# Optimization experiments

Hardware: AMD Instinct MI355X
Metric: run time of the kernel (lower is better)

## Reference

```python
import jax, jax.numpy as jnp
import numpy as np
from jax import lax

B, L_IN, DEC_LEN = 1024, 2048, 64
H = 128            # hidden_size
CARD, EMB = 200, 16  # categorical feature cardinality / embedding dim
VDIM = 4
IN_SIZE = EMB + 1 + 1  # cat-embed + continuous feat (Linear(1,1)) + target value


def setup_inputs() -> dict:
    key = jax.random.key(0)
    k = jax.random.split(key, 19)
    s = 1.0 / np.sqrt(H)  # torch LSTM/Linear default init scale
    u = lambda kk, shape: jax.random.uniform(kk, shape, minval=-s, maxval=s, dtype=jnp.float32)
    return {
        "cat_in": jax.random.randint(k[0], (B, L_IN), 0, CARD, dtype=jnp.int32),
        "cont_in": jax.random.normal(k[1], (B, L_IN, 1), dtype=jnp.float32),
        "X_in": jax.random.normal(k[2], (B, L_IN, 1), dtype=jnp.float32),
        "cat_out": jax.random.randint(k[3], (B, DEC_LEN), 0, CARD, dtype=jnp.int32),
        "cont_out": jax.random.normal(k[4], (B, DEC_LEN, 1), dtype=jnp.float32),
        # learned params
        "emb_table": jax.random.normal(k[5], (CARD, EMB), dtype=jnp.float32) * 0.02,
        "cont_w": jax.random.normal(k[6], (1, 1), dtype=jnp.float32) * 0.5,  # Linear(1,1,bias=False)
        "Wih_e": u(k[7], (4 * H, IN_SIZE)),
        "Whh_e": u(k[8], (4 * H, H)),
        "b_e": u(k[9], (4 * H,)),   # b_ih + b_hh folded together
        "Wih_d": u(k[10], (4 * H, IN_SIZE)),
        "Whh_d": u(k[11], (4 * H, H)),
        "b_d": u(k[12], (4 * H,)),
        "Wm": u(k[13], (1, H)), "bm": u(k[14], (1,)),
        "Ws": u(k[15], (1, H)), "bs": u(k[16], (1,)),
        "Wv": u(k[17], (VDIM, H)), "bv": u(k[18], (VDIM,)),
    }


def _lstm_cell(x, h, c, Wih, Whh, b):
    # torch gate order: i, f, g, o
    gates = x @ Wih.T + h @ Whh.T + b  # [B, 4H]
    i, f, g, o = jnp.split(gates, 4, axis=-1)
    c_new = jax.nn.sigmoid(f) * c + jax.nn.sigmoid(i) * jnp.tanh(g)
    h_new = jax.nn.sigmoid(o) * jnp.tanh(c_new)
    return h_new, c_new


def reference(cat_in, cont_in, X_in, cat_out, cont_out, emb_table, cont_w,
              Wih_e, Whh_e, b_e, Wih_d, Whh_d, b_d, Wm, bm, Ws, bs, Wv, bv):
    w00 = cont_w[0, 0]
    # feature embedding: Embedding for categorical, Linear(1,1,no bias) for continuous
    feats_in_embed = jnp.concatenate([emb_table[cat_in], cont_in * w00], axis=-1)  # [B,L,EMB+1]
    enc_in = jnp.concatenate([feats_in_embed, X_in], axis=-1)                      # [B,L,IN_SIZE]

    h0 = jnp.zeros((X_in.shape[0], H), dtype=X_in.dtype)

    def enc_step(carry, xt):
        h, c = carry
        return _lstm_cell(xt, h, c, Wih_e, Whh_e, b_e), None

    # encoder outputs are unused downstream; only the final (h, c) state matters
    (h, c), _ = lax.scan(enc_step, (h0, h0), jnp.swapaxes(enc_in, 0, 1))

    feats_out_embed = jnp.concatenate([emb_table[cat_out], cont_out * w00], axis=-1)  # [B,D,EMB+1]

    def dec_step(carry, feats_next):
        h, c, x_prev, f_prev = carry
        xt = jnp.concatenate([f_prev, x_prev], axis=-1)  # [B, IN_SIZE]
        h, c = _lstm_cell(xt, h, c, Wih_d, Whh_d, b_d)
        mu = h @ Wm.T + bm                     # [B,1]
        std = jax.nn.softplus(h @ Ws.T + bs)   # [B,1]
        v = h @ Wv.T + bv                      # [B,VDIM]
        return (h, c, mu, feats_next), (mu, std, v)

    init = (h, c, X_in[:, -1, :], feats_in_embed[:, -1, :])
    _, (means, stds, vs) = lax.scan(dec_step, init, jnp.swapaxes(feats_out_embed, 0, 1))
    # [D,B,*] -> [B,D,*]
    return (jnp.swapaxes(means, 0, 1), jnp.swapaxes(stds, 0, 1), jnp.swapaxes(vs, 0, 1))
```

## Files before the change

### kernel.cpp

```cpp
#include <hip/hip_runtime.h>
#include <math.h>

typedef _Float16 half8 __attribute__((ext_vector_type(8)));
typedef float float4v __attribute__((ext_vector_type(4)));

constexpr int Lc   = 2048;
constexpr int DECc = 64;
constexpr int Hc   = 128;
constexpr int EMBc = 16;
constexpr int INc  = 18;
constexpr int NBc  = 4;
constexpr int NTc  = 512;
constexpr int CARD = 200;
constexpr int ZS   = 160;


__device__ __forceinline__ float rcp_(float x) { return __builtin_amdgcn_rcpf(x); }
__device__ __forceinline__ float sigm(float x) { return rcp_(1.0f + __expf(-x)); }
__device__ __forceinline__ float tanh_(float x) { return 2.0f * rcp_(1.0f + __expf(-2.0f * x)) - 1.0f; }
__device__ __forceinline__ float softplus_(float x) { return __logf(1.0f + __expf(x)); }

__device__ __forceinline__ float sel4(float4v v, int q) {
    const float a = (q & 1) ? v[1] : v[0];
    const float b = (q & 1) ? v[3] : v[2];
    return (q & 2) ? b : a;
}


__global__ __launch_bounds__(NTc, 1) void rnnar_kernel(
    const int*   __restrict__ cat_in,  const float* __restrict__ cont_in,
    const float* __restrict__ X_in,    const int*   __restrict__ cat_out,
    const float* __restrict__ cont_out,const float* __restrict__ emb_table,
    const float* __restrict__ cont_w,
    const float* __restrict__ Wih_e, const float* __restrict__ Whh_e, const float* __restrict__ b_e,
    const float* __restrict__ Wih_d, const float* __restrict__ Whh_d, const float* __restrict__ b_d,
    const float* __restrict__ Wm, const float* __restrict__ bm,
    const float* __restrict__ Ws, const float* __restrict__ bs,
    const float* __restrict__ Wv, const float* __restrict__ bv,
    float* __restrict__ out)
{
    __shared__ _Float16      z_lds[2][NBc * ZS];
    __shared__ _Float16      emb_lds[CARD * EMBc];
    __shared__ _Float16      xs0[NBc * Lc];
    __shared__ _Float16      xs1[NBc * Lc];
    __shared__ _Float16      xo_lds[NBc * DECc];
    __shared__ unsigned char catb[NBc * Lc];
    __shared__ unsigned char catob[NBc * DECc];
    __shared__ float         h32_lds[NBc * 132];
    __shared__ float         wh_lds[6 * Hc];
    __shared__ float         hb_lds[8];
    __shared__ float         mu_lds[4];

    const int tid  = threadIdx.x;
    const int lane = tid & 63;
    const int wv   = tid >> 6;
    const int q    = lane >> 4;
    const int col  = lane & 15;
    const int cell = 16 * wv + col;
    const int bx   = col & 3;
    const int b0   = blockIdx.x * NBc;
    const float w00 = cont_w[0];

    {
        int* z32 = (int*)&z_lds[0][0];
        for (int i = tid; i < NBc * ZS; i += NTc) z32[i] = 0;
    }
    for (int i = tid; i < NBc * Lc; i += NTc) {
        const int b = i >> 11, t = i & (Lc - 1);
        catb[i] = (unsigned char)cat_in[(b0 + b) * Lc + t];
        xs0[i]  = (_Float16)(cont_in[(b0 + b) * Lc + t] * w00);
        xs1[i]  = (_Float16)(X_in[(b0 + b) * Lc + t]);
    }
    if (tid < NBc * DECc) {
        const int b = tid >> 6, t = tid & 63;
        catob[tid]  = (unsigned char)cat_out[(b0 + b) * DECc + t];
        xo_lds[tid] = (_Float16)(cont_out[(b0 + b) * DECc + t] * w00);
    }
    for (int i = tid; i < CARD * EMBc; i += NTc) emb_lds[i] = (_Float16)emb_table[i];
    for (int i = tid; i < 6 * Hc; i += NTc) {
        const int o = i >> 7, k = i & 127;
        wh_lds[i] = (o == 0) ? Wm[k] : (o == 1) ? Ws[k] : Wv[(o - 2) * Hc + k];
    }
    if (tid == 0) { hb_lds[0] = bm[0]; hb_lds[1] = bs[0]; }
    if (tid < 4)  { hb_lds[2 + tid] = bv[tid]; mu_lds[tid] = 0.0f; }

    half8 Bf[4][5];
    float bias_s[4];
    float w17_s[4];
    #define LOAD_T(WIH, WHH, BB)                                               \
    {                                                                          \
        _Pragma("unroll")                                                      \
        for (int gt = 0; gt < 4; ++gt) {                                       \
            const int row = gt * Hc + cell;                                    \
            _Pragma("unroll")                                                  \
            for (int kt = 0; kt < 5; ++kt) {                                   \
                half8 f;                                                       \
                _Pragma("unroll")                                              \
                for (int j = 0; j < 8; ++j) {                                  \
                    const int k = 32 * kt + 8 * q + j;                         \
                    float v = 0.0f;                                            \
                    if (k < Hc)             v = WHH[row * Hc + k];             \
                    else if (k < Hc + INc)  v = WIH[row * INc + (k - Hc)];     \
                    f[j] = (_Float16)v;                                        \
                }                                                              \
                Bf[gt][kt] = f;                                                \
            }                                                                  \
            bias_s[gt] = BB[row];                                              \
            w17_s[gt]  = WIH[row * INc + 17];                                  \
        }                                                                      \
    }

    LOAD_T(Wih_e, Whh_e, b_e);
    __syncthreads();

    float4v acc_pre[4];

    #define PRE_ENC(T1)                                                        \
    {                                                                          \
        const int t1 = (T1);                                                   \
        half8 ax;                                                              \
        _Pragma("unroll") for (int j = 0; j < 8; ++j) ax[j] = (_Float16)0.0f;  \
        if (q < 2)       ax = *(const half8*)&emb_lds[(int)catb[bx * Lc + t1] * EMBc + 8 * q]; \
        else if (q == 2) { ax[0] = xs0[bx * Lc + t1]; ax[1] = xs1[bx * Lc + t1]; } \
        _Pragma("unroll")                                                      \
        for (int gt = 0; gt < 4; ++gt) {                                       \
            float4v a = {bias_s[gt], bias_s[gt], bias_s[gt], bias_s[gt]};      \
            acc_pre[gt] = __builtin_amdgcn_mfma_f32_16x16x32_f16(ax, Bf[gt][4], a, 0, 0, 0); \
        }                                                                      \
    }

    PRE_ENC(0);

    int p = 0;
    float c_reg = 0.f;

    for (int t = 0; t < Lc; ++t) {
        const _Float16* zr = &z_lds[p][0];
        _Float16*       zw = &z_lds[p ^ 1][0];

        const _Float16* ap = zr + bx * ZS + 8 * q;
        half8 Az[4];
        #pragma unroll
        for (int kt = 0; kt < 4; ++kt) Az[kt] = *(const half8*)(ap + 32 * kt);

        float4v acc[4];
        #pragma unroll
        for (int gt = 0; gt < 4; ++gt) {
            float4v a = acc_pre[gt];
            #pragma unroll
            for (int kt = 0; kt < 4; ++kt)
                a = __builtin_amdgcn_mfma_f32_16x16x32_f16(Az[kt], Bf[gt][kt], a, 0, 0, 0);
            acc[gt] = a;
        }

        PRE_ENC((t + 1 < Lc) ? t + 1 : Lc - 1);

        const float gi = sel4(acc[0], q);
        const float gf = sel4(acc[1], q);
        const float gg = sel4(acc[2], q);
        const float go = sel4(acc[3], q);

        const float cn = sigm(gf) * c_reg + sigm(gi) * tanh_(gg);
        c_reg = cn;
        zw[q * ZS + cell] = (_Float16)(sigm(go) * tanh_(cn));

        __syncthreads();
        p ^= 1;
    }

    LOAD_T(Wih_d, Whh_d, b_d);
    const float bm0 = hb_lds[0], bs0 = hb_lds[1];

    {
        const int t1 = Lc - 1;
        half8 ax;
        #pragma unroll
        for (int j = 0; j < 8; ++j) ax[j] = (_Float16)0.0f;
        if (q < 2)       ax = *(const half8*)&emb_lds[(int)catb[bx * Lc + t1] * EMBc + 8 * q];
        else if (q == 2) { ax[0] = xs0[bx * Lc + t1]; ax[1] = xs1[bx * Lc + t1]; }
        #pragma unroll
        for (int gt = 0; gt < 4; ++gt) {
            float4v a = {bias_s[gt], bias_s[gt], bias_s[gt], bias_s[gt]};
            acc_pre[gt] = __builtin_amdgcn_mfma_f32_16x16x32_f16(ax, Bf[gt][4], a, 0, 0, 0);
        }
    }
    __syncthreads();

    for (int t = 0; t < DECc; ++t) {
        const _Float16* zr = &z_lds[p][0];
        _Float16*       zw = &z_lds[p ^ 1][0];

        const float muq = mu_lds[q];

        const _Float16* ap = zr + bx * ZS + 8 * q;
        half8 Az[4];
        #pragma unroll
        for (int kt = 0; kt < 4; ++kt) Az[kt] = *(const half8*)(ap + 32 * kt);

        float4v acc[4];
        #pragma unroll
        for (int gt = 0; gt < 4; ++gt) {
            float4v a = acc_pre[gt];
            #pragma unroll
            for (int kt = 0; kt < 4; ++kt)
                a = __builtin_amdgcn_mfma_f32_16x16x32_f16(Az[kt], Bf[gt][kt], a, 0, 0, 0);
            acc[gt] = a;
        }

        {
            half8 ax;
            #pragma unroll
            for (int j = 0; j < 8; ++j) ax[j] = (_Float16)0.0f;
            if (q < 2)       ax = *(const half8*)&emb_lds[(int)catob[bx * DECc + t] * EMBc + 8 * q];
            else if (q == 2) ax[0] = xo_lds[bx * DECc + t];
            #pragma unroll
            for (int gt = 0; gt < 4; ++gt) {
                float4v a = {bias_s[gt], bias_s[gt], bias_s[gt], bias_s[gt]};
                acc_pre[gt] = __builtin_amdgcn_mfma_f32_16x16x32_f16(ax, Bf[gt][4], a, 0, 0, 0);
            }
        }

        const float gi = sel4(acc[0], q) + muq * w17_s[0];
        const float gf = sel4(acc[1], q) + muq * w17_s[1];
        const float gg = sel4(acc[2], q) + muq * w17_s[2];
        const float go = sel4(acc[3], q) + muq * w17_s[3];

        const float cn = sigm(gf) * c_reg + sigm(gi) * tanh_(gg);
        c_reg = cn;
        const float hv = sigm(go) * tanh_(cn);
        zw[q * ZS + cell] = (_Float16)hv;
        h32_lds[q * 132 + cell] = hv;

        __syncthreads();

        if (tid < 384) {
            const int grp = tid >> 4;
            const int l16 = tid & 15;
            const int b   = grp & 3, o = grp >> 2;
            float s = 0.0f;
            #pragma unroll
            for (int j = 0; j < 8; ++j) {
                const int k = l16 + 16 * j;
                s += wh_lds[o * Hc + k] * h32_lds[b * 132 + k];
            }
            s += __shfl_xor(s, 1);
            s += __shfl_xor(s, 2);
            s += __shfl_xor(s, 4);
            s += __shfl_xor(s, 8);
            if (l16 == 0) {
                const int gb = b0 + b;
                if (o == 0) {
                    const float mu = s + bm0;
                    out[gb * DECc + t] = mu;
                    mu_lds[b] = mu;
                } else if (o == 1) {
                    out[65536 + gb * DECc + t] = softplus_(s + bs0);
                } else {
                    out[131072 + (gb * DECc + t) * 4 + (o - 2)] = s + hb_lds[2 + (o - 2)];
                }
            }
        }
        __syncthreads();
        p ^= 1;
    }
    #undef LOAD_T
    #undef PRE_ENC
}

extern "C" void kernel_launch(void* const* d_in, const int* in_sizes, int n_in,
                              void* d_out, int out_size, void* d_ws, size_t ws_size,
                              hipStream_t stream) {
    rnnar_kernel<<<1024 / NBc, NTc, 0, stream>>>(
        (const int*)d_in[0],   (const float*)d_in[1],  (const float*)d_in[2],
        (const int*)d_in[3],   (const float*)d_in[4],  (const float*)d_in[5],
        (const float*)d_in[6],
        (const float*)d_in[7], (const float*)d_in[8],  (const float*)d_in[9],
        (const float*)d_in[10],(const float*)d_in[11], (const float*)d_in[12],
        (const float*)d_in[13],(const float*)d_in[14],
        (const float*)d_in[15],(const float*)d_in[16],
        (const float*)d_in[17],(const float*)d_in[18],
        (float*)d_out);
}
```

Measured before the change: 1.380 ms.

## Stream encoder inputs from global and batch input projections over four timesteps

Drops the up-front staging of the whole 2048-step input sequence into shared memory. Each wave now loads the inputs for four future timesteps from global memory during the loop. One MFMA per gate computes the input-plus-bias projections for four steps by four batches, which are stashed in a small LDS buffer and read back each step. This is meant to shrink the long prologue, the LDS footprint and the per-step input MFMA work. In exchange, global-load latency now sits inside the serial recurrence with only one step of prefetch distance.

```diff
diff --git a/kernel.cpp b/kernel.cpp
--- a/kernel.cpp
+++ b/kernel.cpp
@@ -25,7 +25,6 @@
     const float b = (q & 1) ? v[3] : v[2];
     return (q & 2) ? b : a;
 }
-
 
 __global__ __launch_bounds__(NTc, 1) void rnnar_kernel(
     const int*   __restrict__ cat_in,  const float* __restrict__ cont_in,
@@ -41,15 +40,13 @@
 {
     __shared__ _Float16      z_lds[2][NBc * ZS];
     __shared__ _Float16      emb_lds[CARD * EMBc];
-    __shared__ _Float16      xs0[NBc * Lc];
-    __shared__ _Float16      xs1[NBc * Lc];
-    __shared__ _Float16      xo_lds[NBc * DECc];
-    __shared__ unsigned char catb[NBc * Lc];
-    __shared__ unsigned char catob[NBc * DECc];
+    __shared__ _Float16      xo4[DECc * NBc];
+    __shared__ unsigned char catob4[DECc * NBc];
     __shared__ float         h32_lds[NBc * 132];
     __shared__ float         wh_lds[6 * Hc];
     __shared__ float         hb_lds[8];
     __shared__ float         mu_lds[4];
+    __shared__ float4v       x_lds[8][4][4][16];
 
     const int tid  = threadIdx.x;
     const int lane = tid & 63;
@@ -58,6 +55,8 @@
     const int col  = lane & 15;
     const int cell = 16 * wv + col;
     const int bx   = col & 3;
+    const int gu   = col >> 2;
+    const int gb   = col & 3;
     const int b0   = blockIdx.x * NBc;
     const float w00 = cont_w[0];
 
@@ -65,18 +64,12 @@
         int* z32 = (int*)&z_lds[0][0];
         for (int i = tid; i < NBc * ZS; i += NTc) z32[i] = 0;
     }
-    for (int i = tid; i < NBc * Lc; i += NTc) {
-        const int b = i >> 11, t = i & (Lc - 1);
-        catb[i] = (unsigned char)cat_in[(b0 + b) * Lc + t];
-        xs0[i]  = (_Float16)(cont_in[(b0 + b) * Lc + t] * w00);
-        xs1[i]  = (_Float16)(X_in[(b0 + b) * Lc + t]);
-    }
+    for (int i = tid; i < CARD * EMBc; i += NTc) emb_lds[i] = (_Float16)emb_table[i];
     if (tid < NBc * DECc) {
-        const int b = tid >> 6, t = tid & 63;
-        catob[tid]  = (unsigned char)cat_out[(b0 + b) * DECc + t];
-        xo_lds[tid] = (_Float16)(cont_out[(b0 + b) * DECc + t] * w00);
-    }
-    for (int i = tid; i < CARD * EMBc; i += NTc) emb_lds[i] = (_Float16)emb_table[i];
+        const int t = tid >> 2, b = tid & 3;
+        catob4[tid] = (unsigned char)cat_out[(b0 + b) * DECc + t];
+        xo4[tid]    = (_Float16)(cont_out[(b0 + b) * DECc + t] * w00);
+    }
     for (int i = tid; i < 6 * Hc; i += NTc) {
         const int o = i >> 7, k = i & 127;
         wh_lds[i] = (o == 0) ? Wm[k] : (o == 1) ? Ws[k] : Wv[(o - 2) * Hc + k];
@@ -110,26 +103,35 @@
         }                                                                      \
     }
 
-    LOAD_T(Wih_e, Whh_e, b_e);
-    __syncthreads();
-
-    float4v acc_pre[4];
-
-    #define PRE_ENC(T1)                                                        \
+    #define BUILD_X(GCAT, GCONT, GX)                                           \
     {                                                                          \
-        const int t1 = (T1);                                                   \
         half8 ax;                                                              \
         _Pragma("unroll") for (int j = 0; j < 8; ++j) ax[j] = (_Float16)0.0f;  \
-        if (q < 2)       ax = *(const half8*)&emb_lds[(int)catb[bx * Lc + t1] * EMBc + 8 * q]; \
-        else if (q == 2) { ax[0] = xs0[bx * Lc + t1]; ax[1] = xs1[bx * Lc + t1]; } \
+        if (q < 2)       ax = *(const half8*)&emb_lds[(GCAT) * EMBc + 8 * q];  \
+        else if (q == 2) { ax[0] = (_Float16)((GCONT) * w00); ax[1] = (_Float16)(GX); } \
         _Pragma("unroll")                                                      \
         for (int gt = 0; gt < 4; ++gt) {                                       \
             float4v a = {bias_s[gt], bias_s[gt], bias_s[gt], bias_s[gt]};      \
-            acc_pre[gt] = __builtin_amdgcn_mfma_f32_16x16x32_f16(ax, Bf[gt][4], a, 0, 0, 0); \
+            a = __builtin_amdgcn_mfma_f32_16x16x32_f16(ax, Bf[gt][4], a, 0, 0, 0); \
+            x_lds[wv][q][gt][col] = a;                                         \
         }                                                                      \
     }
 
-    PRE_ENC(0);
+    LOAD_T(Wih_e, Whh_e, b_e);
+    __syncthreads();
+
+    int   g_cat;  float g_cont, g_X;
+    {
+        const long idx = (long)(b0 + gb) * Lc + gu;
+        g_cat  = cat_in[idx];
+        g_cont = cont_in[idx];
+        g_X    = X_in[idx];
+    }
+    BUILD_X(g_cat, g_cont, g_X);
+
+    float4v xinit[4];
+    #pragma unroll
+    for (int gt = 0; gt < 4; ++gt) xinit[gt] = x_lds[wv][0][gt][col];
 
     int p = 0;
     float c_reg = 0.f;
@@ -146,14 +148,26 @@
         float4v acc[4];
         #pragma unroll
         for (int gt = 0; gt < 4; ++gt) {
-            float4v a = acc_pre[gt];
+            float4v a = xinit[gt];
             #pragma unroll
             for (int kt = 0; kt < 4; ++kt)
                 a = __builtin_amdgcn_mfma_f32_16x16x32_f16(Az[kt], Bf[gt][kt], a, 0, 0, 0);
             acc[gt] = a;
         }
 
-        PRE_ENC((t + 1 < Lc) ? t + 1 : Lc - 1);
+        if ((t & 3) == 2 && t + 2 < Lc) {
+            const long idx = (long)(b0 + gb) * Lc + (t + 2 + gu);
+            g_cat  = cat_in[idx];
+            g_cont = cont_in[idx];
+            g_X    = X_in[idx];
+        }
+        if ((t & 3) == 3 && t + 1 < Lc) BUILD_X(g_cat, g_cont, g_X);
+
+        {
+            const int sn = (t + 1) & 3;
+            #pragma unroll
+            for (int gt = 0; gt < 4; ++gt) xinit[gt] = x_lds[wv][sn][gt][col];
+        }
 
         const float gi = sel4(acc[0], q);
         const float gf = sel4(acc[1], q);
@@ -171,13 +185,17 @@
     LOAD_T(Wih_d, Whh_d, b_d);
     const float bm0 = hb_lds[0], bs0 = hb_lds[1];
 
+    float4v acc_pre[4];
     {
-        const int t1 = Lc - 1;
+        const long idx = (long)(b0 + bx) * Lc + (Lc - 1);
+        const int   c0 = cat_in[idx];
+        const float cc = cont_in[idx];
+        const float xx = X_in[idx];
         half8 ax;
         #pragma unroll
         for (int j = 0; j < 8; ++j) ax[j] = (_Float16)0.0f;
-        if (q < 2)       ax = *(const half8*)&emb_lds[(int)catb[bx * Lc + t1] * EMBc + 8 * q];
-        else if (q == 2) { ax[0] = xs0[bx * Lc + t1]; ax[1] = xs1[bx * Lc + t1]; }
+        if (q < 2)       ax = *(const half8*)&emb_lds[c0 * EMBc + 8 * q];
+        else if (q == 2) { ax[0] = (_Float16)(cc * w00); ax[1] = (_Float16)xx; }
         #pragma unroll
         for (int gt = 0; gt < 4; ++gt) {
             float4v a = {bias_s[gt], bias_s[gt], bias_s[gt], bias_s[gt]};
@@ -211,8 +229,8 @@
             half8 ax;
             #pragma unroll
             for (int j = 0; j < 8; ++j) ax[j] = (_Float16)0.0f;
-            if (q < 2)       ax = *(const half8*)&emb_lds[(int)catob[bx * DECc + t] * EMBc + 8 * q];
-            else if (q == 2) ax[0] = xo_lds[bx * DECc + t];
+            if (q < 2)       ax = *(const half8*)&emb_lds[(int)catob4[t * 4 + bx] * EMBc + 8 * q];
+            else if (q == 2) ax[0] = xo4[t * 4 + bx];
             #pragma unroll
             for (int gt = 0; gt < 4; ++gt) {
                 float4v a = {bias_s[gt], bias_s[gt], bias_s[gt], bias_s[gt]};
@@ -248,15 +266,15 @@
             s += __shfl_xor(s, 4);
             s += __shfl_xor(s, 8);
             if (l16 == 0) {
-                const int gb = b0 + b;
+                const int gb2 = b0 + b;
                 if (o == 0) {
                     const float mu = s + bm0;
-                    out[gb * DECc + t] = mu;
+                    out[gb2 * DECc + t] = mu;
                     mu_lds[b] = mu;
                 } else if (o == 1) {
-                    out[65536 + gb * DECc + t] = softplus_(s + bs0);
+                    out[65536 + gb2 * DECc + t] = softplus_(s + bs0);
                 } else {
-                    out[131072 + (gb * DECc + t) * 4 + (o - 2)] = s + hb_lds[2 + (o - 2)];
+                    out[131072 + (gb2 * DECc + t) * 4 + (o - 2)] = s + hb_lds[2 + (o - 2)];
                 }
             }
         }
@@ -264,7 +282,7 @@
         p ^= 1;
     }
     #undef LOAD_T
-    #undef PRE_ENC
+    #undef BUILD_X
 }
 
 extern "C" void kernel_launch(void* const* d_in, const int* in_sizes, int n_in,
```

Measured after the change: 1.244 ms. -9.8%, faster.
